# Optimization experiments

Measured on AMD Instinct MI355X. Metric: run time of the kernel, lower is better.

## Reference

```python
import jax, jax.numpy as jnp
import numpy as np

B, T, H, C = 32, 256, 128, 3
KL, KS = 500, 10
IN3 = C * 3  # 9 channels after concat


def conv1d(x, w, b):
    # x: [B, C, L], w: [O, I, K], b: [O]; torch Conv1d VALID, stride 1
    y = jax.lax.conv_general_dilated(x, w, window_strides=(1,), padding='VALID',
                                     dimension_numbers=('NCH', 'OIH', 'NCH'))
    return y + b[None, :, None]


def setup_inputs() -> dict:
    key = jax.random.key(0)
    ks = jax.random.split(key, 20)
    s = 0.05  # parameter scale to keep activations numerically sane
    f32 = jnp.float32
    return {
        'input1': jax.random.normal(ks[0], (B, T + KL - 1, C), f32),
        'input2': jax.random.normal(ks[1], (B, T + KS - 1, C), f32),
        'input3': jax.random.normal(ks[2], (B, T, C), f32),
        'h': jnp.zeros((B, H), f32),
        'W_ih': jax.random.normal(ks[3], (H, IN3), f32) * s,
        'W_hh': jax.random.normal(ks[4], (H, H), f32) * s,
        'b_h': jax.random.normal(ks[5], (H,), f32) * s,
        'W_ho': jax.random.normal(ks[6], (H, H), f32) * s,
        'b_o': jax.random.normal(ks[7], (H,), f32) * s,
        'conv_l_w': jax.random.normal(ks[8], (C, C, KL), f32) * s,
        'conv_l_b': jax.random.normal(ks[9], (C,), f32) * s,
        'conv_s_w': jax.random.normal(ks[10], (C, C, KS), f32) * s,
        'conv_s_b': jax.random.normal(ks[11], (C,), f32) * s,
        't_k': jax.random.normal(ks[12], (1, H, H), f32) * s,
        't_v': jax.random.normal(ks[13], (1, H, H), f32) * s,
        't_q': jax.random.normal(ks[14], (1, H, H), f32) * s,
        'Wm0': jax.random.normal(ks[15], (H, H), f32) * s,
        'bm0': jax.random.normal(ks[16], (H,), f32) * s,
        'out_W': jax.random.normal(ks[17], (1, H), f32) * s,
        'out_b': jax.random.normal(ks[18], (1,), f32) * s,
    }


def reference(input1, input2, input3, h, W_ih, W_hh, b_h, W_ho, b_o,
              conv_l_w, conv_l_b, conv_s_w, conv_s_b, t_k, t_v, t_q,
              Wm0, bm0, out_W, out_b):
    # conv feature extraction (torch: permute to [B,C,L])
    x_l = conv1d(jnp.transpose(input1, (0, 2, 1)), conv_l_w, conv_l_b)  # [B,C,T]
    x_s = conv1d(jnp.transpose(input2, (0, 2, 1)), conv_s_w, conv_s_b)  # [B,C,T]
    x = jnp.concatenate([x_l, x_s, jnp.transpose(input3, (0, 2, 1))], axis=1)  # [B,9,T]
    x = jnp.transpose(x, (0, 2, 1))  # [B,T,9]

    tk, tv, tq = t_k[0], t_v[0], t_q[0]
    hb = h @ W_hh.T + b_h  # h is never updated -> constant over time

    lr, b1, b2, eps = 0.01, 0.9, 0.999, 1e-8

    def step(carry, x_t):
        Wm, bm, mW, vW, mb, vb, t = carry
        out_t = x_t @ W_ih.T + hb                 # [B,H]
        trv = out_t @ tk                          # train view [B,H]
        lbl = out_t @ tv                          # label view [B,H]
        pred = trv @ Wm.T + bm
        g = (2.0 / pred.size) * (pred - lbl)      # dMSE/dpred
        gW = g.T @ trv                            # dL/dWm [H,H]
        gb = g.sum(0)                             # dL/dbm [H]
        t = t + 1.0
        mW = b1 * mW + (1 - b1) * gW
        vW = b2 * vW + (1 - b2) * gW * gW
        mb = b1 * mb + (1 - b1) * gb
        vb = b2 * vb + (1 - b2) * gb * gb
        bc1 = 1.0 - b1 ** t
        bc2 = 1.0 - b2 ** t
        Wm = Wm - lr * (mW / bc1) / (jnp.sqrt(vW / bc2) + eps)
        bm = bm - lr * (mb / bc1) / (jnp.sqrt(vb / bc2) + eps)
        hi = (out_t @ tq) @ Wm.T + bm             # predict with updated fast weights
        y = hi @ W_ho.T + b_o
        return (Wm, bm, mW, vW, mb, vb, t), y

    init = (Wm0, bm0, jnp.zeros_like(Wm0), jnp.zeros_like(Wm0),
            jnp.zeros_like(bm0), jnp.zeros_like(bm0), jnp.float32(0.0))
    _, ys = jax.lax.scan(step, init, jnp.transpose(x, (1, 0, 2)))  # ys: [T,B,H]
    out = ys[-1] @ out_W.T + out_b  # only last timestep feeds out_layer
    return (out, h)
```

## Files before the change

kernel.cpp:

```cpp
#include <hip/hip_runtime.h>
#include <math.h>

#define B_ 32
#define T_ 256
#define H_ 128
#define KL_ 500
#define KS_ 10

typedef _Float16 h8 __attribute__((ext_vector_type(8)));
typedef _Float16 h2 __attribute__((ext_vector_type(2)));

__global__ void k_front(const float* __restrict__ in1, const float* __restrict__ in2,
                        const float* __restrict__ wl, const float* __restrict__ bl,
                        const float* __restrict__ ws, const float* __restrict__ bs,
                        const float* __restrict__ h, const float* __restrict__ Whh,
                        const float* __restrict__ bh,
                        float* __restrict__ xf, float* __restrict__ hb,
                        float* __restrict__ dout) {
    int b = blockIdx.x, oc = blockIdx.y;
    int t = threadIdx.x;
    if (oc == 6) {
        __shared__ float hrow[128];
        if (t < 128) hrow[t] = h[b * 128 + t];
        __syncthreads();
        if (t < 128) {
            float acc = bh[t];
            #pragma unroll 4
            for (int k = 0; k < 128; ++k) acc += hrow[k] * Whh[t * 128 + k];
            hb[b * 128 + t] = acc;
            dout[32 + b * 128 + t] = hrow[t];
        }
        return;
    }
    __shared__ float s_in[755 * 3];
    __shared__ float s_w[3 * KL_];
    if (oc < 3) {
        int o = oc;
        for (int i = t; i < 755 * 3; i += 256) s_in[i] = in1[b * 755 * 3 + i];
        for (int i = t; i < 3 * KL_; i += 256) s_w[i] = wl[o * 3 * KL_ + i];
        __syncthreads();
        float acc = bl[o];
        for (int i = 0; i < 3; ++i) {
            const float* wrow = &s_w[i * KL_];
            #pragma unroll 4
            for (int k = 0; k < KL_; ++k)
                acc += s_in[(t + k) * 3 + i] * wrow[k];
        }
        xf[(b * T_ + t) * 6 + o] = acc;
    } else {
        int o = oc - 3;
        for (int i = t; i < 265 * 3; i += 256) s_in[i] = in2[b * 265 * 3 + i];
        for (int i = t; i < 3 * KS_; i += 256) s_w[i] = ws[o * 3 * KS_ + i];
        __syncthreads();
        float acc = bs[o];
        for (int i = 0; i < 3; ++i) {
            #pragma unroll
            for (int k = 0; k < KS_; ++k)
                acc += s_in[(t + k) * 3 + i] * s_w[i * KS_ + k];
        }
        xf[(b * T_ + t) * 6 + 3 + o] = acc;
    }
}

#define TSTR 136

__global__ void k_feat(const float* __restrict__ xf, const float* __restrict__ in3,
                       const float* __restrict__ hb, const float* __restrict__ Wih,
                       const float* __restrict__ tk, const float* __restrict__ tv,
                       const float* __restrict__ tq,
                       _Float16* __restrict__ rwP, _Float16* __restrict__ clP,
                       float* __restrict__ lblT, float* __restrict__ outq) {
    int t = blockIdx.x;
    int tid = threadIdx.x;
    const int hh = tid & 127;
    const int grp = tid >> 7;
    const bool last = (t == T_ - 1);

    __shared__ __align__(16) _Float16 tkT[128 * TSTR];
    __shared__ __align__(16) _Float16 tvT[128 * TSTR];
    __shared__ __align__(16) _Float16 tqT[128 * TSTR];
    __shared__ __align__(16) float out_s[B_ * H_];

    for (int j = 0; j < 8; ++j) {
        int idx = j * 512 + tid;
        int b = idx >> 7, hx = idx & 127;
        const float* w = &Wih[hx * 9];
        const float* x6 = &xf[(b * T_ + t) * 6];
        const float* x3 = &in3[(b * T_ + t) * 3];
        float acc = hb[idx];
        acc += x6[0] * w[0] + x6[1] * w[1] + x6[2] * w[2]
             + x6[3] * w[3] + x6[4] * w[4] + x6[5] * w[5]
             + x3[0] * w[6] + x3[1] * w[7] + x3[2] * w[8];
        out_s[idx] = acc;
    }
    for (int i = tid; i < 16384; i += 512) {
        int k = i >> 7, hx = i & 127;
        tkT[hx * TSTR + k] = (_Float16)tk[i];
        tvT[hx * TSTR + k] = (_Float16)tv[i];
    }
    if (last) {
        for (int i = tid; i < 16384; i += 512) {
            int k = i >> 7, hx = i & 127;
            tqT[hx * TSTR + k] = (_Float16)tq[i];
        }
    }
    __syncthreads();

    float a_tr[8], a_lb[8], a_tq[8];
    #pragma unroll
    for (int o = 0; o < 8; ++o) { a_tr[o] = 0.f; a_lb[o] = 0.f; a_tq[o] = 0.f; }

    for (int kc = 0; kc < 8; ++kc) {
        const int4* tk4 = (const int4*)&tkT[hh * TSTR + kc * 16];
        const int4* tv4 = (const int4*)&tvT[hh * TSTR + kc * 16];
        h8 ka = __builtin_bit_cast(h8, tk4[0]), kb = __builtin_bit_cast(h8, tk4[1]);
        h8 va = __builtin_bit_cast(h8, tv4[0]), vb = __builtin_bit_cast(h8, tv4[1]);
        h8 qa, qb;
        if (last) {
            const int4* tq4 = (const int4*)&tqT[hh * TSTR + kc * 16];
            qa = __builtin_bit_cast(h8, tq4[0]); qb = __builtin_bit_cast(h8, tq4[1]);
        }
        #pragma unroll
        for (int o = 0; o < 8; ++o) {
            int b = o * 4 + grp;
            const float4* os4 = (const float4*)&out_s[b * 128 + kc * 16];
            float4 q0 = os4[0], q1 = os4[1], q2 = os4[2], q3 = os4[3];
            float osv[16] = {q0.x, q0.y, q0.z, q0.w, q1.x, q1.y, q1.z, q1.w,
                             q2.x, q2.y, q2.z, q2.w, q3.x, q3.y, q3.z, q3.w};
            #pragma unroll
            for (int k2 = 0; k2 < 8; ++k2) {
                a_tr[o] = fmaf(osv[k2], (float)ka[k2], a_tr[o]);
                a_lb[o] = fmaf(osv[k2], (float)va[k2], a_lb[o]);
                if (last) a_tq[o] = fmaf(osv[k2], (float)qa[k2], a_tq[o]);
            }
            #pragma unroll
            for (int k2 = 0; k2 < 8; ++k2) {
                a_tr[o] = fmaf(osv[8 + k2], (float)kb[k2], a_tr[o]);
                a_lb[o] = fmaf(osv[8 + k2], (float)vb[k2], a_lb[o]);
                if (last) a_tq[o] = fmaf(osv[8 + k2], (float)qb[k2], a_tq[o]);
            }
        }
    }

    for (int o = 0; o < 8; ++o) {
        int b = o * 4 + grp;
        _Float16 v16 = (_Float16)a_tr[o];
        int p = hh & 63;
        rwP[t * 4096 + ((p >> 3) << 9) + ((2 * b + (hh >> 6)) << 3) + (p & 7)] = v16;
        int q = ((hh & 1) << 5) + b;
        clP[t * 4096 + ((q >> 3) << 9) + ((hh >> 1) << 3) + (q & 7)] = v16;
        lblT[t * 4096 + hh * 32 + b] = a_lb[o];
        if (last) outq[b * 128 + hh] = a_tq[o];
    }
}

#define DPP_ADD(S, CTRL)                                                           \
  do { int _d = __builtin_amdgcn_update_dpp(0, __float_as_int(S), (CTRL), 0xF,     \
                                            0xF, true);                            \
       (S) += __int_as_float(_d); } while (0)

#if __has_builtin(__builtin_amdgcn_fdot2)
#define FDOT2(ci, gi, acc)                                                         \
  __builtin_amdgcn_fdot2(__builtin_bit_cast(h2, (ci)),                             \
                         __builtin_bit_cast(h2, (gi)), (acc), false)
#else
static __device__ __forceinline__ float fdot2_sw(int a, int b, float c) {
    h2 ha = __builtin_bit_cast(h2, a), hb2 = __builtin_bit_cast(h2, b);
    return fmaf((float)ha.y, (float)hb2.y, fmaf((float)ha.x, (float)hb2.x, c));
}
#define FDOT2(ci, gi, acc) fdot2_sw((ci), (gi), (acc))
#endif

__global__
__attribute__((amdgpu_flat_work_group_size(64, 64), amdgpu_waves_per_eu(1, 1)))
void k_scan(
    const _Float16* __restrict__ rwP, const _Float16* __restrict__ clP,
    const float* __restrict__ lblT,
    const float* __restrict__ Wm0, const float* __restrict__ bm0,
    const float* __restrict__ outq, float* __restrict__ hi_ws) {
    const int h = blockIdx.x;
    const int lane = threadIdx.x;
    const int row = lane >> 1;
    const int hf = lane & 1;
    const int hf32i = hf * 32;
    const int lblidx = h * 32 + row;

    __shared__ __align__(16) int w16[64];
    __shared__ __align__(16) float ew[128];

    float2 wv = *(const float2*)&Wm0[h * 128 + 2 * lane];
    float w0 = wv.x, w1 = wv.y;
    float mW0 = 0.f, vW0 = 0.f, mW1 = 0.f, vW1 = 0.f;
    float bm = bm0[h];
    float mb = 0.f, vb = 0.f, pb1 = 1.f, pb2 = 1.f;

    w16[lane] = __builtin_bit_cast(int, __builtin_amdgcn_cvt_pkrtz(w0, w1));

    h8 rw[8], cl[8];
    float lbl;
    {
        const h8* rs = (const h8*)(rwP);
        const h8* cs = (const h8*)(clP);
        #pragma unroll
        for (int j = 0; j < 8; ++j) rw[j] = rs[j * 64 + lane];
        #pragma unroll
        for (int j = 0; j < 8; ++j) cl[j] = cs[j * 64 + lane];
        lbl = lblT[lblidx];
    }

    const float cg = 2.0f / 4096.0f;
    const float lr = 0.01f, BB1 = 0.9f, BB2 = 0.999f;
    const float OB1 = 0.1f, OB2 = 0.001f;
    const float SEPS = 1e-16f;

    for (int t = 0; t < T_; ++t) {
        pb1 *= BB1; pb2 *= BB2;
        const float na = (-lr) * __builtin_amdgcn_sqrtf(1.0f - pb2) *
                         __builtin_amdgcn_rcpf(1.0f - pb1);
        const int tpre = (t + 1 < T_) ? (t + 1) : (T_ - 1);

        float g;
        {
            float f0 = 0.f, f1 = 0.f, f2 = 0.f, f3 = 0.f;
            #pragma unroll
            for (int j = 0; j < 8; ++j) {
                int4 xj = __builtin_bit_cast(int4, rw[j]);
                int4 wj = *(const int4*)&w16[hf32i + 4 * j];
                f0 = FDOT2(xj.x, wj.x, f0); f1 = FDOT2(xj.y, wj.y, f1);
                f2 = FDOT2(xj.z, wj.z, f2); f3 = FDOT2(xj.w, wj.w, f3);
            }
            float pp = (f0 + f2) + (f1 + f3);
            int po = __builtin_amdgcn_update_dpp(0, __float_as_int(pp), 0xB1, 0xF, 0xF, true);
            g = (pp + __int_as_float(po)) + bm - lbl;
        }

        {
            const h8* rs = (const h8*)(rwP + (size_t)tpre * 4096);
            #pragma unroll
            for (int j = 0; j < 8; ++j) rw[j] = rs[j * 64 + lane];
            lbl = lblT[(size_t)tpre * 4096 + lblidx];
        }

        int pkg;
        {
            int gnb = __builtin_amdgcn_update_dpp(0, __float_as_int(g), 0x4E, 0xF, 0xF, true);
            pkg = __builtin_bit_cast(int,
                __builtin_amdgcn_cvt_pkrtz(g, __int_as_float(gnb)));
        }
        float gsum = g;
        DPP_ADD(gsum, 0x4E); DPP_ADD(gsum, 0x124); DPP_ADD(gsum, 0x128);
        gsum += __shfl_xor(gsum, 16); gsum += __shfl_xor(gsum, 32);

        int gp[16];
        #pragma unroll
        for (int i = 0; i < 16; ++i)
            gp[i] = __builtin_amdgcn_readlane(pkg, 4 * i);

        float gk0, gk1;
        {
            float f0 = 0.f, f1 = 0.f, f2 = 0.f, f3 = 0.f;
            float f4 = 0.f, f5 = 0.f, f6 = 0.f, f7 = 0.f;
            #pragma unroll
            for (int j = 0; j < 4; ++j) {
                int4 cj = __builtin_bit_cast(int4, cl[j]);
                f0 = FDOT2(cj.x, gp[4 * j + 0], f0); f1 = FDOT2(cj.y, gp[4 * j + 1], f1);
                f2 = FDOT2(cj.z, gp[4 * j + 2], f2); f3 = FDOT2(cj.w, gp[4 * j + 3], f3);
            }
            #pragma unroll
            for (int j = 0; j < 4; ++j) {
                int4 cj = __builtin_bit_cast(int4, cl[j + 4]);
                f4 = FDOT2(cj.x, gp[4 * j + 0], f4); f5 = FDOT2(cj.y, gp[4 * j + 1], f5);
                f6 = FDOT2(cj.z, gp[4 * j + 2], f6); f7 = FDOT2(cj.w, gp[4 * j + 3], f7);
            }
            gk0 = cg * ((f0 + f2) + (f1 + f3));
            gk1 = cg * ((f4 + f6) + (f5 + f7));
        }

        {
            const h8* cs = (const h8*)(clP + (size_t)tpre * 4096);
            #pragma unroll
            for (int j = 0; j < 8; ++j) cl[j] = cs[j * 64 + lane];
        }

        mW0 = fmaf(BB1, mW0, OB1 * gk0);
        vW0 = fmaf(BB2, vW0, OB2 * gk0 * gk0);
        w0 = fmaf(mW0 * __builtin_amdgcn_rsqf(vW0 + SEPS), na, w0);
        mW1 = fmaf(BB1, mW1, OB1 * gk1);
        vW1 = fmaf(BB2, vW1, OB2 * gk1 * gk1);
        w1 = fmaf(mW1 * __builtin_amdgcn_rsqf(vW1 + SEPS), na, w1);

        w16[lane] = __builtin_bit_cast(int, __builtin_amdgcn_cvt_pkrtz(w0, w1));

        {
            float gb = cg * gsum;
            mb = fmaf(BB1, mb, OB1 * gb);
            vb = fmaf(BB2, vb, OB2 * gb * gb);
            bm = fmaf(mb * __builtin_amdgcn_rsqf(vb + SEPS), na, bm);
        }
    }

    *(float2*)&ew[2 * lane] = make_float2(w0, w1);
    {
        const int rowbase = row * 128 + hf * 64;
        float a0 = 0.f, a1 = 0.f, a2 = 0.f, a3 = 0.f;
        #pragma unroll
        for (int j = 0; j < 16; ++j) {
            float4 xv = ((const float4*)(outq + rowbase))[j];
            float4 wv4 = *(const float4*)&ew[hf * 64 + 4 * j];
            a0 = fmaf(xv.x, wv4.x, a0); a1 = fmaf(xv.y, wv4.y, a1);
            a2 = fmaf(xv.z, wv4.z, a2); a3 = fmaf(xv.w, wv4.w, a3);
        }
        float pp = (a0 + a2) + (a1 + a3);
        int po = __builtin_amdgcn_update_dpp(0, __float_as_int(pp), 0xB1, 0xF, 0xF, true);
        float pred = pp + __int_as_float(po);
        if (hf == 0) hi_ws[row * 128 + h] = pred + bm;
    }
}

__global__ void k_out(const float* __restrict__ hi, const float* __restrict__ Who,
                      const float* __restrict__ bo, const float* __restrict__ outW,
                      const float* __restrict__ outb, float* __restrict__ dout) {
    int b = blockIdx.x, hh = threadIdx.x;
    __shared__ float hrow[128];
    __shared__ float part[2];
    hrow[hh] = hi[b * 128 + hh];
    __syncthreads();
    float acc = bo[hh];
    #pragma unroll 4
    for (int k = 0; k < 128; ++k) acc += hrow[k] * Who[hh * 128 + k];
    float v = acc * outW[hh];
    v += __shfl_down(v, 32, 64);
    v += __shfl_down(v, 16, 64);
    v += __shfl_down(v, 8, 64);
    v += __shfl_down(v, 4, 64);
    v += __shfl_down(v, 2, 64);
    v += __shfl_down(v, 1, 64);
    if ((hh & 63) == 0) part[hh >> 6] = v;
    __syncthreads();
    if (hh == 0) dout[b] = part[0] + part[1] + outb[0];
}

extern "C" void kernel_launch(void* const* d_in, const int* in_sizes, int n_in,
                              void* d_out, int out_size, void* d_ws, size_t ws_size,
                              hipStream_t stream) {
    (void)in_sizes; (void)n_in; (void)out_size; (void)ws_size;
    const float* in1   = (const float*)d_in[0];
    const float* in2   = (const float*)d_in[1];
    const float* in3   = (const float*)d_in[2];
    const float* h     = (const float*)d_in[3];
    const float* Wih   = (const float*)d_in[4];
    const float* Whh   = (const float*)d_in[5];
    const float* bh    = (const float*)d_in[6];
    const float* Who   = (const float*)d_in[7];
    const float* bo    = (const float*)d_in[8];
    const float* wl    = (const float*)d_in[9];
    const float* bl    = (const float*)d_in[10];
    const float* wsc   = (const float*)d_in[11];
    const float* bsc   = (const float*)d_in[12];
    const float* tk    = (const float*)d_in[13];
    const float* tv    = (const float*)d_in[14];
    const float* tq    = (const float*)d_in[15];
    const float* Wm0   = (const float*)d_in[16];
    const float* bm0   = (const float*)d_in[17];
    const float* outW  = (const float*)d_in[18];
    const float* outb  = (const float*)d_in[19];
    float* out = (float*)d_out;

    float* wsf = (float*)d_ws;
    float*    xf    = wsf;
    float*    hb    = wsf + 49152;
    _Float16* rwH   = (_Float16*)(wsf + 53248);
    _Float16* clH   = (_Float16*)(wsf + 53248 + 524288);
    float*    lblT  = wsf + 53248 + 1048576;
    float*    outq  = wsf + 53248 + 2097152;
    float*    hi_ws = wsf + 53248 + 2101248;

    k_front<<<dim3(32, 7), 256, 0, stream>>>(in1, in2, wl, bl, wsc, bsc,
                                             h, Whh, bh, xf, hb, out);
    k_feat<<<256, 512, 0, stream>>>(xf, in3, hb, Wih, tk, tv, tq,
                                    rwH, clH, lblT, outq);
    k_scan<<<128, 64, 0, stream>>>(rwH, clH, lblT, Wm0, bm0, outq, hi_ws);
    k_out<<<32, 128, 0, stream>>>(hi_ws, Who, bo, outW, outb, out);
}
```

Baseline: 198.0 us.

## Shorten scan critical path: precompute Adam step table, fold scales, move final projections

Precomputes the per-step Adam bias-correction factor into a table in the front kernel. The gradient scale cg is folded into the moment constants and epsilon so the scan drops a multiply per step. The loop is manually unrolled by two, and the bias minus label term is formed ahead of time. The tq projection and final prediction move out of k_feat and k_scan into k_out, shortening the serial scan tail. In exchange k_out does more serial work, and the folded epsilon slightly changes numerics.

```diff
diff --git a/kernel.cpp b/kernel.cpp
--- a/kernel.cpp
+++ b/kernel.cpp
@@ -16,9 +16,15 @@
                         const float* __restrict__ h, const float* __restrict__ Whh,
                         const float* __restrict__ bh,
                         float* __restrict__ xf, float* __restrict__ hb,
-                        float* __restrict__ dout) {
+                        float* __restrict__ naT, float* __restrict__ dout) {
     int b = blockIdx.x, oc = blockIdx.y;
     int t = threadIdx.x;
+    if (oc == 7) {
+        if (b == 0)
+            naT[t] = -0.01f * sqrtf(1.0f - powf(0.999f, (float)(t + 1)))
+                           / (1.0f - powf(0.9f, (float)(t + 1)));
+        return;
+    }
     if (oc == 6) {
         __shared__ float hrow[128];
         if (t < 128) hrow[t] = h[b * 128 + t];
@@ -67,18 +73,15 @@
 __global__ void k_feat(const float* __restrict__ xf, const float* __restrict__ in3,
                        const float* __restrict__ hb, const float* __restrict__ Wih,
                        const float* __restrict__ tk, const float* __restrict__ tv,
-                       const float* __restrict__ tq,
                        _Float16* __restrict__ rwP, _Float16* __restrict__ clP,
-                       float* __restrict__ lblT, float* __restrict__ outq) {
+                       float* __restrict__ lblT, float* __restrict__ o255) {
     int t = blockIdx.x;
     int tid = threadIdx.x;
     const int hh = tid & 127;
     const int grp = tid >> 7;
-    const bool last = (t == T_ - 1);
 
     __shared__ __align__(16) _Float16 tkT[128 * TSTR];
     __shared__ __align__(16) _Float16 tvT[128 * TSTR];
-    __shared__ __align__(16) _Float16 tqT[128 * TSTR];
     __shared__ __align__(16) float out_s[B_ * H_];
 
     for (int j = 0; j < 8; ++j) {
@@ -98,28 +101,21 @@
         tkT[hx * TSTR + k] = (_Float16)tk[i];
         tvT[hx * TSTR + k] = (_Float16)tv[i];
     }
-    if (last) {
-        for (int i = tid; i < 16384; i += 512) {
-            int k = i >> 7, hx = i & 127;
-            tqT[hx * TSTR + k] = (_Float16)tq[i];
-        }
-    }
-    __syncthreads();
-
-    float a_tr[8], a_lb[8], a_tq[8];
+    __syncthreads();
+
+    if (t == T_ - 1) {
+        for (int j = 0; j < 8; ++j) o255[j * 512 + tid] = out_s[j * 512 + tid];
+    }
+
+    float a_tr[8], a_lb[8];
     #pragma unroll
-    for (int o = 0; o < 8; ++o) { a_tr[o] = 0.f; a_lb[o] = 0.f; a_tq[o] = 0.f; }
+    for (int o = 0; o < 8; ++o) { a_tr[o] = 0.f; a_lb[o] = 0.f; }
 
     for (int kc = 0; kc < 8; ++kc) {
         const int4* tk4 = (const int4*)&tkT[hh * TSTR + kc * 16];
         const int4* tv4 = (const int4*)&tvT[hh * TSTR + kc * 16];
         h8 ka = __builtin_bit_cast(h8, tk4[0]), kb = __builtin_bit_cast(h8, tk4[1]);
         h8 va = __builtin_bit_cast(h8, tv4[0]), vb = __builtin_bit_cast(h8, tv4[1]);
-        h8 qa, qb;
-        if (last) {
-            const int4* tq4 = (const int4*)&tqT[hh * TSTR + kc * 16];
-            qa = __builtin_bit_cast(h8, tq4[0]); qb = __builtin_bit_cast(h8, tq4[1]);
-        }
         #pragma unroll
         for (int o = 0; o < 8; ++o) {
             int b = o * 4 + grp;
@@ -131,13 +127,11 @@
             for (int k2 = 0; k2 < 8; ++k2) {
                 a_tr[o] = fmaf(osv[k2], (float)ka[k2], a_tr[o]);
                 a_lb[o] = fmaf(osv[k2], (float)va[k2], a_lb[o]);
-                if (last) a_tq[o] = fmaf(osv[k2], (float)qa[k2], a_tq[o]);
             }
             #pragma unroll
             for (int k2 = 0; k2 < 8; ++k2) {
                 a_tr[o] = fmaf(osv[8 + k2], (float)kb[k2], a_tr[o]);
                 a_lb[o] = fmaf(osv[8 + k2], (float)vb[k2], a_lb[o]);
-                if (last) a_tq[o] = fmaf(osv[8 + k2], (float)qb[k2], a_tq[o]);
             }
         }
     }
@@ -150,7 +144,6 @@
         int q = ((hh & 1) << 5) + b;
         clP[t * 4096 + ((q >> 3) << 9) + ((hh >> 1) << 3) + (q & 7)] = v16;
         lblT[t * 4096 + hh * 32 + b] = a_lb[o];
-        if (last) outq[b * 128 + hh] = a_tq[o];
     }
 }
 
@@ -171,33 +164,117 @@
 #define FDOT2(ci, gi, acc) fdot2_sw((ci), (gi), (acc))
 #endif
 
+#define SCAN_STEP(TT)                                                              \
+  do {                                                                             \
+    const int tpre = ((TT) + 1 < T_) ? ((TT) + 1) : (T_ - 1);                      \
+                                \
+    float g;                                                                       \
+    {                                                                              \
+      float f0 = 0.f, f1 = 0.f, f2 = 0.f, f3 = 0.f;                                \
+      _Pragma("unroll")                                                            \
+      for (int j = 0; j < 8; ++j) {                                                \
+        int4 xj = __builtin_bit_cast(int4, rw[j]);                                 \
+        int4 wj = *(const int4*)&w16[hf32i + 4 * j];                               \
+        f0 = FDOT2(xj.x, wj.x, f0); f1 = FDOT2(xj.y, wj.y, f1);                    \
+        f2 = FDOT2(xj.z, wj.z, f2); f3 = FDOT2(xj.w, wj.w, f3);                    \
+      }                                                                            \
+      float pp = (f0 + f2) + (f1 + f3);                                            \
+      int po = __builtin_amdgcn_update_dpp(0, __float_as_int(pp), 0xB1, 0xF, 0xF,  \
+                                           true);                                  \
+      g = (pp + __int_as_float(po)) + bml;                      \
+    }                                                                              \
+                                            \
+    float lbln, nan_;                                                              \
+    {                                                                              \
+      const h8* rs = (const h8*)(rwP + (size_t)tpre * 4096);                       \
+      _Pragma("unroll")                                                            \
+      for (int j = 0; j < 8; ++j) rw[j] = rs[j * 64 + lane];                       \
+      lbln = lblT[(size_t)tpre * 4096 + lblidx];                                   \
+      nan_ = naT[tpre];                                                            \
+    }                                                                              \
+                                            \
+    int pkg;                                                                       \
+    {                                                                              \
+      int gnb = __builtin_amdgcn_update_dpp(0, __float_as_int(g), 0x4E, 0xF, 0xF,  \
+                                            true);                                 \
+      pkg = __builtin_bit_cast(int,                                                \
+          __builtin_amdgcn_cvt_pkrtz(g, __int_as_float(gnb)));                     \
+    }                                                                              \
+                     \
+    float gsum = g;                                                                \
+    DPP_ADD(gsum, 0x4E); DPP_ADD(gsum, 0x124); DPP_ADD(gsum, 0x128);               \
+    gsum += __shfl_xor(gsum, 16); gsum += __shfl_xor(gsum, 32);                    \
+                                                          \
+    int gp[16];                                                                    \
+    _Pragma("unroll")                                                              \
+    for (int i = 0; i < 16; ++i)                                                   \
+      gp[i] = __builtin_amdgcn_readlane(pkg, 4 * i);                               \
+                      \
+    float d0, d1;                                                                  \
+    {                                                                              \
+      float f0 = 0.f, f1 = 0.f, f2 = 0.f, f3 = 0.f;                                \
+      float f4 = 0.f, f5 = 0.f, f6 = 0.f, f7 = 0.f;                                \
+      _Pragma("unroll")                                                            \
+      for (int j = 0; j < 4; ++j) {                                                \
+        int4 cj = __builtin_bit_cast(int4, cl[j]);                                 \
+        f0 = FDOT2(cj.x, gp[4 * j + 0], f0); f1 = FDOT2(cj.y, gp[4 * j + 1], f1);  \
+        f2 = FDOT2(cj.z, gp[4 * j + 2], f2); f3 = FDOT2(cj.w, gp[4 * j + 3], f3);  \
+      }                                                                            \
+      _Pragma("unroll")                                                            \
+      for (int j = 0; j < 4; ++j) {                                                \
+        int4 cj = __builtin_bit_cast(int4, cl[j + 4]);                             \
+        f4 = FDOT2(cj.x, gp[4 * j + 0], f4); f5 = FDOT2(cj.y, gp[4 * j + 1], f5);  \
+        f6 = FDOT2(cj.z, gp[4 * j + 2], f6); f7 = FDOT2(cj.w, gp[4 * j + 3], f7);  \
+      }                                                                            \
+      d0 = (f0 + f2) + (f1 + f3);                                                  \
+      d1 = (f4 + f6) + (f5 + f7);                                                  \
+    }                                                                              \
+                                                       \
+    {                                                                              \
+      const h8* cs = (const h8*)(clP + (size_t)tpre * 4096);                       \
+      _Pragma("unroll")                                                            \
+      for (int j = 0; j < 8; ++j) cl[j] = cs[j * 64 + lane];                       \
+    }                                                                              \
+                                            \
+    mW0 = fmaf(BB1, mW0, OB1c * d0);                                               \
+    vW0 = fmaf(BB2, vW0, OB2c * d0 * d0);                                          \
+    w0 = fmaf(mW0 * __builtin_amdgcn_rsqf(vW0 + SEPSW), nav, w0);                  \
+    mW1 = fmaf(BB1, mW1, OB1c * d1);                                               \
+    vW1 = fmaf(BB2, vW1, OB2c * d1 * d1);                                          \
+    w1 = fmaf(mW1 * __builtin_amdgcn_rsqf(vW1 + SEPSW), nav, w1);                  \
+    w16[lane] = __builtin_bit_cast(int, __builtin_amdgcn_cvt_pkrtz(w0, w1));       \
+                 \
+    mb = fmaf(BB1, mb, OB1c * gsum);                                               \
+    vb = fmaf(BB2, vb, OB2c * gsum * gsum);                                        \
+    bm = fmaf(mb * __builtin_amdgcn_rsqf(vb + SEPSW), nav, bm);                    \
+    bml = bm - lbln;                                                               \
+    nav = nan_;                                                                    \
+  } while (0)
+
 __global__
 __attribute__((amdgpu_flat_work_group_size(64, 64), amdgpu_waves_per_eu(1, 1)))
 void k_scan(
     const _Float16* __restrict__ rwP, const _Float16* __restrict__ clP,
-    const float* __restrict__ lblT,
+    const float* __restrict__ lblT, const float* __restrict__ naT,
     const float* __restrict__ Wm0, const float* __restrict__ bm0,
-    const float* __restrict__ outq, float* __restrict__ hi_ws) {
+    float* __restrict__ wfinT, float* __restrict__ bmfin) {
     const int h = blockIdx.x;
     const int lane = threadIdx.x;
-    const int row = lane >> 1;
-    const int hf = lane & 1;
-    const int hf32i = hf * 32;
-    const int lblidx = h * 32 + row;
+    const int hf32i = (lane & 1) * 32;
+    const int lblidx = h * 32 + (lane >> 1);
 
     __shared__ __align__(16) int w16[64];
-    __shared__ __align__(16) float ew[128];
 
     float2 wv = *(const float2*)&Wm0[h * 128 + 2 * lane];
     float w0 = wv.x, w1 = wv.y;
     float mW0 = 0.f, vW0 = 0.f, mW1 = 0.f, vW1 = 0.f;
     float bm = bm0[h];
-    float mb = 0.f, vb = 0.f, pb1 = 1.f, pb2 = 1.f;
+    float mb = 0.f, vb = 0.f;
 
     w16[lane] = __builtin_bit_cast(int, __builtin_amdgcn_cvt_pkrtz(w0, w1));
 
     h8 rw[8], cl[8];
-    float lbl;
+    float bml, nav;
     {
         const h8* rs = (const h8*)(rwP);
         const h8* cs = (const h8*)(clP);
@@ -205,129 +282,50 @@
         for (int j = 0; j < 8; ++j) rw[j] = rs[j * 64 + lane];
         #pragma unroll
         for (int j = 0; j < 8; ++j) cl[j] = cs[j * 64 + lane];
-        lbl = lblT[lblidx];
+        bml = bm - lblT[lblidx];
+        nav = naT[0];
     }
 
     const float cg = 2.0f / 4096.0f;
-    const float lr = 0.01f, BB1 = 0.9f, BB2 = 0.999f;
-    const float OB1 = 0.1f, OB2 = 0.001f;
-    const float SEPS = 1e-16f;
-
-    for (int t = 0; t < T_; ++t) {
-        pb1 *= BB1; pb2 *= BB2;
-        const float na = (-lr) * __builtin_amdgcn_sqrtf(1.0f - pb2) *
-                         __builtin_amdgcn_rcpf(1.0f - pb1);
-        const int tpre = (t + 1 < T_) ? (t + 1) : (T_ - 1);
-
-        float g;
-        {
-            float f0 = 0.f, f1 = 0.f, f2 = 0.f, f3 = 0.f;
-            #pragma unroll
-            for (int j = 0; j < 8; ++j) {
-                int4 xj = __builtin_bit_cast(int4, rw[j]);
-                int4 wj = *(const int4*)&w16[hf32i + 4 * j];
-                f0 = FDOT2(xj.x, wj.x, f0); f1 = FDOT2(xj.y, wj.y, f1);
-                f2 = FDOT2(xj.z, wj.z, f2); f3 = FDOT2(xj.w, wj.w, f3);
-            }
-            float pp = (f0 + f2) + (f1 + f3);
-            int po = __builtin_amdgcn_update_dpp(0, __float_as_int(pp), 0xB1, 0xF, 0xF, true);
-            g = (pp + __int_as_float(po)) + bm - lbl;
-        }
-
-        {
-            const h8* rs = (const h8*)(rwP + (size_t)tpre * 4096);
-            #pragma unroll
-            for (int j = 0; j < 8; ++j) rw[j] = rs[j * 64 + lane];
-            lbl = lblT[(size_t)tpre * 4096 + lblidx];
-        }
-
-        int pkg;
-        {
-            int gnb = __builtin_amdgcn_update_dpp(0, __float_as_int(g), 0x4E, 0xF, 0xF, true);
-            pkg = __builtin_bit_cast(int,
-                __builtin_amdgcn_cvt_pkrtz(g, __int_as_float(gnb)));
-        }
-        float gsum = g;
-        DPP_ADD(gsum, 0x4E); DPP_ADD(gsum, 0x124); DPP_ADD(gsum, 0x128);
-        gsum += __shfl_xor(gsum, 16); gsum += __shfl_xor(gsum, 32);
-
-        int gp[16];
-        #pragma unroll
-        for (int i = 0; i < 16; ++i)
-            gp[i] = __builtin_amdgcn_readlane(pkg, 4 * i);
-
-        float gk0, gk1;
-        {
-            float f0 = 0.f, f1 = 0.f, f2 = 0.f, f3 = 0.f;
-            float f4 = 0.f, f5 = 0.f, f6 = 0.f, f7 = 0.f;
-            #pragma unroll
-            for (int j = 0; j < 4; ++j) {
-                int4 cj = __builtin_bit_cast(int4, cl[j]);
-                f0 = FDOT2(cj.x, gp[4 * j + 0], f0); f1 = FDOT2(cj.y, gp[4 * j + 1], f1);
-                f2 = FDOT2(cj.z, gp[4 * j + 2], f2); f3 = FDOT2(cj.w, gp[4 * j + 3], f3);
-            }
-            #pragma unroll
-            for (int j = 0; j < 4; ++j) {
-                int4 cj = __builtin_bit_cast(int4, cl[j + 4]);
-                f4 = FDOT2(cj.x, gp[4 * j + 0], f4); f5 = FDOT2(cj.y, gp[4 * j + 1], f5);
-                f6 = FDOT2(cj.z, gp[4 * j + 2], f6); f7 = FDOT2(cj.w, gp[4 * j + 3], f7);
-            }
-            gk0 = cg * ((f0 + f2) + (f1 + f3));
-            gk1 = cg * ((f4 + f6) + (f5 + f7));
-        }
-
-        {
-            const h8* cs = (const h8*)(clP + (size_t)tpre * 4096);
-            #pragma unroll
-            for (int j = 0; j < 8; ++j) cl[j] = cs[j * 64 + lane];
-        }
-
-        mW0 = fmaf(BB1, mW0, OB1 * gk0);
-        vW0 = fmaf(BB2, vW0, OB2 * gk0 * gk0);
-        w0 = fmaf(mW0 * __builtin_amdgcn_rsqf(vW0 + SEPS), na, w0);
-        mW1 = fmaf(BB1, mW1, OB1 * gk1);
-        vW1 = fmaf(BB2, vW1, OB2 * gk1 * gk1);
-        w1 = fmaf(mW1 * __builtin_amdgcn_rsqf(vW1 + SEPS), na, w1);
-
-        w16[lane] = __builtin_bit_cast(int, __builtin_amdgcn_cvt_pkrtz(w0, w1));
-
-        {
-            float gb = cg * gsum;
-            mb = fmaf(BB1, mb, OB1 * gb);
-            vb = fmaf(BB2, vb, OB2 * gb * gb);
-            bm = fmaf(mb * __builtin_amdgcn_rsqf(vb + SEPS), na, bm);
-        }
-    }
-
-    *(float2*)&ew[2 * lane] = make_float2(w0, w1);
-    {
-        const int rowbase = row * 128 + hf * 64;
-        float a0 = 0.f, a1 = 0.f, a2 = 0.f, a3 = 0.f;
-        #pragma unroll
-        for (int j = 0; j < 16; ++j) {
-            float4 xv = ((const float4*)(outq + rowbase))[j];
-            float4 wv4 = *(const float4*)&ew[hf * 64 + 4 * j];
-            a0 = fmaf(xv.x, wv4.x, a0); a1 = fmaf(xv.y, wv4.y, a1);
-            a2 = fmaf(xv.z, wv4.z, a2); a3 = fmaf(xv.w, wv4.w, a3);
-        }
-        float pp = (a0 + a2) + (a1 + a3);
-        int po = __builtin_amdgcn_update_dpp(0, __float_as_int(pp), 0xB1, 0xF, 0xF, true);
-        float pred = pp + __int_as_float(po);
-        if (hf == 0) hi_ws[row * 128 + h] = pred + bm;
-    }
-}
-
-__global__ void k_out(const float* __restrict__ hi, const float* __restrict__ Who,
-                      const float* __restrict__ bo, const float* __restrict__ outW,
-                      const float* __restrict__ outb, float* __restrict__ dout) {
+    const float BB1 = 0.9f, BB2 = 0.999f;
+    const float OB1c = 0.1f * cg;
+    const float OB2c = 0.001f * cg * cg;
+    const float SEPSW = 1e-16f * cg * cg;
+
+    for (int t = 0; t < T_; t += 2) {
+        SCAN_STEP(t);
+        SCAN_STEP(t + 1);
+    }
+
+    wfinT[(2 * lane) * 128 + h] = w0;
+    wfinT[(2 * lane + 1) * 128 + h] = w1;
+    if (lane == 0) bmfin[h] = bm;
+}
+
+__global__ void k_out(const float* __restrict__ o255, const float* __restrict__ tq,
+                      const float* __restrict__ wfinT, const float* __restrict__ bmfin,
+                      const float* __restrict__ Who, const float* __restrict__ bo,
+                      const float* __restrict__ outW, const float* __restrict__ outb,
+                      float* __restrict__ dout) {
     int b = blockIdx.x, hh = threadIdx.x;
-    __shared__ float hrow[128];
+    __shared__ float o255s[128], oqs[128], his[128];
     __shared__ float part[2];
-    hrow[hh] = hi[b * 128 + hh];
+
+    o255s[hh] = o255[b * 128 + hh];
+    __syncthreads();
+    float oq = 0.f;
+    #pragma unroll 4
+    for (int k = 0; k < 128; ++k) oq = fmaf(o255s[k], tq[k * 128 + hh], oq);
+    oqs[hh] = oq;
+    __syncthreads();
+    float hi = bmfin[hh];
+    #pragma unroll 4
+    for (int k = 0; k < 128; ++k) hi = fmaf(oqs[k], wfinT[k * 128 + hh], hi);
+    his[hh] = hi;
     __syncthreads();
     float acc = bo[hh];
     #pragma unroll 4
-    for (int k = 0; k < 128; ++k) acc += hrow[k] * Who[hh * 128 + k];
+    for (int k = 0; k < 128; ++k) acc = fmaf(his[k], Who[hh * 128 + k], acc);
     float v = acc * outW[hh];
     v += __shfl_down(v, 32, 64);
     v += __shfl_down(v, 16, 64);
@@ -372,13 +370,15 @@
     _Float16* rwH   = (_Float16*)(wsf + 53248);
     _Float16* clH   = (_Float16*)(wsf + 53248 + 524288);
     float*    lblT  = wsf + 53248 + 1048576;
-    float*    outq  = wsf + 53248 + 2097152;
-    float*    hi_ws = wsf + 53248 + 2101248;
-
-    k_front<<<dim3(32, 7), 256, 0, stream>>>(in1, in2, wl, bl, wsc, bsc,
-                                             h, Whh, bh, xf, hb, out);
-    k_feat<<<256, 512, 0, stream>>>(xf, in3, hb, Wih, tk, tv, tq,
-                                    rwH, clH, lblT, outq);
-    k_scan<<<128, 64, 0, stream>>>(rwH, clH, lblT, Wm0, bm0, outq, hi_ws);
-    k_out<<<32, 128, 0, stream>>>(hi_ws, Who, bo, outW, outb, out);
-}
+    float*    naT   = wsf + 53248 + 2097152;
+    float*    o255  = wsf + 53248 + 2097408;
+    float*    wfinT = wsf + 53248 + 2101504;
+    float*    bmfin = wsf + 53248 + 2117888;
+
+    k_front<<<dim3(32, 8), 256, 0, stream>>>(in1, in2, wl, bl, wsc, bsc,
+                                             h, Whh, bh, xf, hb, naT, out);
+    k_feat<<<256, 512, 0, stream>>>(xf, in3, hb, Wih, tk, tv,
+                                    rwH, clH, lblT, o255);
+    k_scan<<<128, 64, 0, stream>>>(rwH, clH, lblT, naT, Wm0, bm0, wfinT, bmfin);
+    k_out<<<32, 128, 0, stream>>>(o255, tq, wfinT, bmfin, Who, bo, outW, outb, out);
+}
```

Result: faster. 174.0 us (-12.1%).
